# Performance work log

Hardware: AMD Instinct MI355X
Metric: run time of the kernel (lower is better)

Reference implementation:

```python
import jax, jax.numpy as jnp
import numpy as np

IN_F = 1024
HID_F = 4096
OUT_F = 1024
B = 64
D = 768
SPARSE_RATIO = 0.1


def setup_inputs() -> dict:
    key = jax.random.key(0)
    k_x, k_w1, k_w2, k_b, k_m = jax.random.split(key, 5)
    # x: [batch, tokens(d), in_features(s)]
    x = jax.random.normal(k_x, (B, D, IN_F), dtype=jnp.float32)
    # scale weights like typical init so GELU inputs stay in a sane range
    fc1_w = jax.random.normal(k_w1, (HID_F, IN_F), dtype=jnp.float32) * (1.0 / np.sqrt(IN_F))
    fc2_w = jax.random.normal(k_w2, (OUT_F, HID_F), dtype=jnp.float32) * (1.0 / np.sqrt(HID_F))
    fc2_b = jax.random.normal(k_b, (OUT_F,), dtype=jnp.float32) * 0.02
    sparse_mask = (jax.random.uniform(k_m, (IN_F, OUT_F)) < SPARSE_RATIO).astype(jnp.float32)
    return {"x": x, "fc1_w": fc1_w, "fc2_w": fc2_w, "fc2_b": fc2_b, "sparse_mask": sparse_mask}


def reference(x, fc1_w, fc2_w, fc2_b, sparse_mask):
    # attn_s[s,t] = sum_d fc1_w[d,s] * fc2_w[t,d] + fc2_b[t]   -> [in, out]
    attn = (jnp.einsum('ds,td->st', fc1_w, fc2_w) + fc2_b) * sparse_mask
    # dropout with p=0.0 is the identity
    out = jnp.einsum('bds,st->bdt', x, attn)  # [B, D, out]
    # torch nn.GELU default is the exact (erf) variant
    return jax.nn.gelu(out, approximate=False)
```

## Files before the change

kernel.cpp:

```cpp
#include <hip/hip_runtime.h>
#include <hip/hip_bf16.h>
#include <math.h>

typedef __attribute__((ext_vector_type(8))) short  short8;
typedef __attribute__((ext_vector_type(4))) float  floatx4;

__device__ __forceinline__ ushort f2bf(float f) {
    __hip_bfloat16 hb = __float2bfloat16(f);
    return *(ushort*)&hb;
}
__device__ __forceinline__ short8 pack8(float4 a, float4 b) {
    union { short8 v; ushort u[8]; } r;
    r.u[0] = f2bf(a.x); r.u[1] = f2bf(a.y); r.u[2] = f2bf(a.z); r.u[3] = f2bf(a.w);
    r.u[4] = f2bf(b.x); r.u[5] = f2bf(b.y); r.u[6] = f2bf(b.z); r.u[7] = f2bf(b.w);
    return r.v;
}

typedef __attribute__((address_space(1))) const void* gas1_t;
typedef __attribute__((address_space(3))) void*       las3_t;
__device__ __forceinline__ void gload16(const void* g, void* l) {
    __builtin_amdgcn_global_load_lds((gas1_t)g, (las3_t)l, 16, 0, 0);
}

__global__ __launch_bounds__(256) void k_cvt(const float* __restrict__ in,
                                             ushort* __restrict__ out, int n8) {
    int i = blockIdx.x * 256 + threadIdx.x;
    if (i >= n8) return;
    const float4* p = reinterpret_cast<const float4*>(in) + (size_t)i * 2;
    float4 a = p[0], b = p[1];
    *reinterpret_cast<short8*>(out + (size_t)i * 8) = pack8(a, b);
}

__global__ __launch_bounds__(256) void k_transpose(const float* __restrict__ in,
                                                   ushort* __restrict__ out) {
    __shared__ float sm[64][65];
    const int tid = threadIdx.x;
    const int s0 = blockIdx.x * 64;
    const int d0 = blockIdx.y * 64;
#pragma unroll
    for (int i = 0; i < 4; ++i) {
        int lin = i * 256 + tid;
        int dr  = lin >> 4;
        int sc4 = lin & 15;
        float4 v = *reinterpret_cast<const float4*>(&in[(size_t)(d0 + dr) * 1024 + s0 + sc4 * 4]);
        sm[dr][sc4 * 4 + 0] = v.x; sm[dr][sc4 * 4 + 1] = v.y;
        sm[dr][sc4 * 4 + 2] = v.z; sm[dr][sc4 * 4 + 3] = v.w;
    }
    __syncthreads();
#pragma unroll
    for (int i = 0; i < 8; ++i) {
        int lin = i * 256 + tid;
        int dc2 = lin & 31;
        int sr  = lin >> 5;
        uint lo = (uint)f2bf(sm[dc2 * 2][sr]);
        uint hi = (uint)f2bf(sm[dc2 * 2 + 1][sr]);
        *reinterpret_cast<uint*>(&out[(size_t)(s0 + sr) * 4096 + d0 + dc2 * 2]) = lo | (hi << 16);
    }
}

template <int BM, int BN, int EPI, int SWZ>
__global__ __launch_bounds__(256) void k_gemm_b(const ushort* __restrict__ A,
                                                const ushort* __restrict__ B,
                                                const float* __restrict__ bias,
                                                const float* __restrict__ mask,
                                                void* __restrict__ Cout,
                                                int lda, int ldb, int ksteps) {
    __shared__ ushort As[BM * 32];
    __shared__ ushort Bs[BN * 32];
    const int tid  = threadIdx.x;
    const int wave = tid >> 6, lane = tid & 63;
    const int wm = wave >> 1, wn = wave & 1;
    const int quad = lane >> 4, m16 = lane & 15;

    int bx = blockIdx.x, by = blockIdx.y;
    if (SWZ) {
        const int nx   = gridDim.x;
        const int nwg  = nx * gridDim.y;
        const int orig = by * nx + bx;
        const int cpx  = nwg >> 3;
        const int w    = (orig & 7) * cpx + (orig >> 3);
        bx = w % nx; by = w / nx;
    }
    const int n0 = bx * BN;
    const int m0 = by * BM;

    constexpr int AI = BM / 32;
    constexpr int BJ = BN / 32;
    floatx4 acc[AI][BJ];
    const floatx4 zero = {0.f, 0.f, 0.f, 0.f};
#pragma unroll
    for (int i = 0; i < AI; ++i)
#pragma unroll
        for (int j = 0; j < BJ; ++j) acc[i][j] = zero;

    const int gr = lane >> 2;
    const int gc = (lane & 3) * 8;

    for (int kt = 0; kt < ksteps; ++kt) {
        const int k0 = kt * 32;
        if (kt) __syncthreads();
#pragma unroll
        for (int t = 0; t < BM / 64; ++t) {
            const int r = wave * (BM / 4) + t * 16;
            gload16(&A[(size_t)(m0 + r + gr) * lda + k0 + gc], &As[r * 32]);
        }
#pragma unroll
        for (int t = 0; t < BN / 64; ++t) {
            const int r = wave * (BN / 4) + t * 16;
            gload16(&B[(size_t)(n0 + r + gr) * ldb + k0 + gc], &Bs[r * 32]);
        }
        __syncthreads();

        short8 aF[AI], bF[BJ];
#pragma unroll
        for (int i = 0; i < AI; ++i)
            aF[i] = *reinterpret_cast<const short8*>(&As[(wm * (BM / 2) + i * 16 + m16) * 32 + quad * 8]);
#pragma unroll
        for (int j = 0; j < BJ; ++j)
            bF[j] = *reinterpret_cast<const short8*>(&Bs[(wn * (BN / 2) + j * 16 + m16) * 32 + quad * 8]);
#pragma unroll
        for (int i = 0; i < AI; ++i)
#pragma unroll
            for (int j = 0; j < BJ; ++j)
                acc[i][j] = __builtin_amdgcn_mfma_f32_16x16x32_bf16(aF[i], bF[j], acc[i][j], 0, 0, 0);
    }

#pragma unroll
    for (int i = 0; i < AI; ++i) {
#pragma unroll
        for (int j = 0; j < BJ; ++j) {
            const int col = n0 + wn * (BN / 2) + j * 16 + m16;
            float bv = 0.f;
            if (EPI == 0) bv = bias[col];
#pragma unroll
            for (int rr = 0; rr < 4; ++rr) {
                const int row = m0 + wm * (BM / 2) + i * 16 + quad * 4 + rr;
                float v = acc[i][j][rr];
                if (EPI == 0) {
                    v = (v + bv) * mask[(size_t)row * 1024 + col];
                    ((ushort*)Cout)[(size_t)col * 1024 + row] = f2bf(v);
                } else {
                    float g = 0.5f * v * (1.0f + erff(v * 0.70710678118654752f));
                    ((float*)Cout)[(size_t)row * 1024 + col] = g;
                }
            }
        }
    }
}

__global__ __launch_bounds__(256) void k_gemm_f32a(const float* __restrict__ Af,
                                                   const ushort* __restrict__ B,
                                                   float* __restrict__ Cout,
                                                   int lda, int ldb, int ksteps) {
    __shared__ ushort As[128 * 32];
    __shared__ ushort Bs[128 * 32];
    const int tid  = threadIdx.x;
    const int wave = tid >> 6, lane = tid & 63;
    const int wm = wave >> 1, wn = wave & 1;
    const int quad = lane >> 4, m16 = lane & 15;
    const int n0 = blockIdx.x * 128;
    const int m0 = blockIdx.y * 128;

    floatx4 acc[4][4];
    const floatx4 zero = {0.f, 0.f, 0.f, 0.f};
#pragma unroll
    for (int i = 0; i < 4; ++i)
#pragma unroll
        for (int j = 0; j < 4; ++j) acc[i][j] = zero;

    const int s_r = tid >> 2;
    const int s_c = tid & 3;
    const int gr = lane >> 2;
    const int gc = (lane & 3) * 8;

    for (int kt = 0; kt < ksteps; ++kt) {
        const int k0 = kt * 32;
        const float* r0 = &Af[(size_t)(m0 + s_r) * lda + k0 + s_c * 8];
        const float* r1 = &Af[(size_t)(m0 + 64 + s_r) * lda + k0 + s_c * 8];
        short8 a0 = pack8(*reinterpret_cast<const float4*>(r0), *reinterpret_cast<const float4*>(r0 + 4));
        short8 a1 = pack8(*reinterpret_cast<const float4*>(r1), *reinterpret_cast<const float4*>(r1 + 4));
        __syncthreads();
        *reinterpret_cast<short8*>(&As[(s_r)      * 32 + s_c * 8]) = a0;
        *reinterpret_cast<short8*>(&As[(64 + s_r) * 32 + s_c * 8]) = a1;
#pragma unroll
        for (int t = 0; t < 2; ++t) {
            const int r = wave * 32 + t * 16;
            gload16(&B[(size_t)(n0 + r + gr) * ldb + k0 + gc], &Bs[r * 32]);
        }
        __syncthreads();

        short8 aF[4], bF[4];
#pragma unroll
        for (int i = 0; i < 4; ++i)
            aF[i] = *reinterpret_cast<const short8*>(&As[(wm * 64 + i * 16 + m16) * 32 + quad * 8]);
#pragma unroll
        for (int j = 0; j < 4; ++j)
            bF[j] = *reinterpret_cast<const short8*>(&Bs[(wn * 64 + j * 16 + m16) * 32 + quad * 8]);
#pragma unroll
        for (int i = 0; i < 4; ++i)
#pragma unroll
            for (int j = 0; j < 4; ++j)
                acc[i][j] = __builtin_amdgcn_mfma_f32_16x16x32_bf16(aF[i], bF[j], acc[i][j], 0, 0, 0);
    }

#pragma unroll
    for (int i = 0; i < 4; ++i)
#pragma unroll
        for (int j = 0; j < 4; ++j) {
            const int col = n0 + wn * 64 + j * 16 + m16;
#pragma unroll
            for (int rr = 0; rr < 4; ++rr) {
                const int row = m0 + wm * 64 + i * 16 + quad * 4 + rr;
                float v = acc[i][j][rr];
                Cout[(size_t)row * 1024 + col] = 0.5f * v * (1.0f + erff(v * 0.70710678118654752f));
            }
        }
}

extern "C" void kernel_launch(void* const* d_in, const int* in_sizes, int n_in,
                              void* d_out, int out_size, void* d_ws, size_t ws_size,
                              hipStream_t stream) {
    const float* x    = (const float*)d_in[0];
    const float* fc1w = (const float*)d_in[1];
    const float* fc2w = (const float*)d_in[2];
    const float* fc2b = (const float*)d_in[3];
    const float* mask = (const float*)d_in[4];

    char* ws = (char*)d_ws;
    ushort* fc1T  = (ushort*)ws;
    ushort* fc2wb = (ushort*)(ws + (8u  << 20));
    ushort* attnT = (ushort*)(ws + (16u << 20));
    ushort* xb    = (ushort*)(ws + (18u << 20));
    const size_t XB_BYTES = 50331648ull * 2;
    const bool has_xb = ws_size >= (size_t)(18u << 20) + XB_BYTES;

    k_transpose<<<dim3(16, 64), 256, 0, stream>>>(fc1w, fc1T);
    k_cvt<<<2048, 256, 0, stream>>>(fc2w, fc2wb, 524288);
    k_gemm_b<64, 64, 0, 1><<<dim3(16, 16), 256, 0, stream>>>(
        fc1T, fc2wb, fc2b, mask, attnT, 4096, 4096, 128);
    if (has_xb) {
        k_cvt<<<24576, 256, 0, stream>>>(x, xb, 6291456);
        k_gemm_b<128, 128, 1, 1><<<dim3(8, 384), 256, 0, stream>>>(
            xb, attnT, nullptr, nullptr, d_out, 1024, 1024, 32);
    } else {
        k_gemm_f32a<<<dim3(8, 384), 256, 0, stream>>>(x, attnT, (float*)d_out, 1024, 1024, 32);
    }
}
```

Measured before the change: 559.9 us.

## Split-K the attn GEMM and add a pipelined 256x256 main GEMM kernel

The small attn GEMM (K=4096, only 256 blocks) becomes a 4-way split-K with a separate reduction kernel that applies bias, mask and the transpose to bf16, so more of the GPU is busy. The main x@attn GEMM is replaced with a 512-thread kernel that uses 256x256 tiles, swizzled LDS, double-buffered global_load_lds staging, and hand-scheduled barriers, waitcnts and setprio so loads overlap with MFMA. This adds an fp32 partial buffer round trip and a fragile hand pipeline in exchange for higher MFMA utilisation.

```diff
diff --git a/kernel.cpp b/kernel.cpp
--- a/kernel.cpp
+++ b/kernel.cpp
@@ -4,6 +4,7 @@
 
 typedef __attribute__((ext_vector_type(8))) short  short8;
 typedef __attribute__((ext_vector_type(4))) float  floatx4;
+typedef __attribute__((ext_vector_type(4))) int    i32x4;
 
 __device__ __forceinline__ ushort f2bf(float f) {
     __hip_bfloat16 hb = __float2bfloat16(f);
@@ -20,6 +21,11 @@
 typedef __attribute__((address_space(3))) void*       las3_t;
 __device__ __forceinline__ void gload16(const void* g, void* l) {
     __builtin_amdgcn_global_load_lds((gas1_t)g, (las3_t)l, 16, 0, 0);
+}
+__device__ __forceinline__ short8 ds_read16(uint off) {
+    union { i32x4 i; short8 s; } u;
+    asm volatile("ds_read_b128 %0, %1" : "=v"(u.i) : "v"(off));
+    return u.s;
 }
 
 __global__ __launch_bounds__(256) void k_cvt(const float* __restrict__ in,
@@ -72,6 +78,13 @@
     const int wm = wave >> 1, wn = wave & 1;
     const int quad = lane >> 4, m16 = lane & 15;
 
+    if (EPI == 2) {
+        const int sp = blockIdx.z;
+        A += (size_t)sp * 1024;
+        B += (size_t)sp * 1024;
+        Cout = (void*)((float*)Cout + (size_t)sp * 1048576);
+    }
+
     int bx = blockIdx.x, by = blockIdx.y;
     if (SWZ) {
         const int nx   = gridDim.x;
@@ -139,10 +152,161 @@
                 if (EPI == 0) {
                     v = (v + bv) * mask[(size_t)row * 1024 + col];
                     ((ushort*)Cout)[(size_t)col * 1024 + row] = f2bf(v);
-                } else {
+                } else if (EPI == 1) {
                     float g = 0.5f * v * (1.0f + erff(v * 0.70710678118654752f));
                     ((float*)Cout)[(size_t)row * 1024 + col] = g;
+                } else {
+                    ((float*)Cout)[(size_t)col * 1024 + row] = v;
                 }
+            }
+        }
+    }
+}
+
+__global__ __launch_bounds__(256) void k_attn_fin(const float* __restrict__ P,
+                                                  const float* __restrict__ bias,
+                                                  const float* __restrict__ mask,
+                                                  ushort* __restrict__ attnT) {
+    const int idx = blockIdx.x * 256 + threadIdx.x;
+    const int t  = idx >> 7;
+    const int s0 = (idx & 127) << 3;
+    float s[8];
+#pragma unroll
+    for (int j = 0; j < 8; ++j) s[j] = 0.f;
+#pragma unroll
+    for (int sp = 0; sp < 4; ++sp) {
+        const float4* p = reinterpret_cast<const float4*>(&P[(size_t)sp * 1048576 + (size_t)t * 1024 + s0]);
+        float4 a = p[0], b = p[1];
+        s[0] += a.x; s[1] += a.y; s[2] += a.z; s[3] += a.w;
+        s[4] += b.x; s[5] += b.y; s[6] += b.z; s[7] += b.w;
+    }
+    const float bv = bias[t];
+    union { short8 v; ushort u[8]; } r;
+#pragma unroll
+    for (int j = 0; j < 8; ++j) {
+        float v = (s[j] + bv) * mask[(size_t)(s0 + j) * 1024 + t];
+        r.u[j] = f2bf(v);
+    }
+    *reinterpret_cast<short8*>(&attnT[(size_t)t * 1024 + s0]) = r.v;
+}
+
+#define GPH(T_, C_, KS_, MH_, RDB_, NB_)                                         \
+  do {                                                                           \
+    _Pragma("unroll")                                                            \
+    for (int i_ = 0; i_ < 4; ++i_)                                               \
+      aA[i_] = ds_read16(bA_ + (uint)((KS_) * 16384 + ((MH_) * 4 + i_) * 1024)); \
+    if (RDB_) {                                                                  \
+      _Pragma("unroll")                                                          \
+      for (int j_ = 0; j_ < 4; ++j_)                                             \
+        bB[j_] = ds_read16(bB_ + (uint)((KS_) * 16384 + j_ * 1024));             \
+    }                                                                            \
+    stage_ht(4 * (T_) + (C_) + 5);                                               \
+    __builtin_amdgcn_sched_barrier(0);                                           \
+    __builtin_amdgcn_s_barrier();                                                \
+    asm volatile("s_waitcnt lgkmcnt(0)");                                        \
+    __builtin_amdgcn_sched_barrier(0);                                           \
+    __builtin_amdgcn_s_setprio(1);                                               \
+    _Pragma("unroll")                                                            \
+    for (int i_ = 0; i_ < 4; ++i_) {                                             \
+      _Pragma("unroll")                                                          \
+      for (int j_ = 0; j_ < 4; ++j_)                                             \
+        acc[(MH_) * 4 + i_][j_] = __builtin_amdgcn_mfma_f32_16x16x32_bf16(       \
+            aA[i_], bB[j_], acc[(MH_) * 4 + i_][j_], 0, 0, 0);                   \
+    }                                                                            \
+    __builtin_amdgcn_s_setprio(0);                                               \
+    __builtin_amdgcn_sched_barrier(0);                                           \
+    if ((NB_) >= 0) {                                                            \
+      if ((NB_) == 4) asm volatile("s_waitcnt vmcnt(4)");                        \
+      else            asm volatile("s_waitcnt vmcnt(0)");                        \
+      __builtin_amdgcn_sched_barrier(0);                                         \
+    }                                                                            \
+    __builtin_amdgcn_s_barrier();                                                \
+    __builtin_amdgcn_sched_barrier(0);                                           \
+  } while (0)
+
+__global__ __launch_bounds__(512) void k_gemm8(const ushort* __restrict__ A,
+                                               const ushort* __restrict__ B,
+                                               float* __restrict__ C) {
+    constexpr int NT = 16;
+    __shared__ __align__(16) ushort lds[65536];
+
+    const int tid  = threadIdx.x;
+    const int wave = tid >> 6, lane = tid & 63;
+    const int wm = wave >> 2, wn = wave & 3;
+    const int quad = lane >> 4, m16 = lane & 15;
+
+    const int orig = blockIdx.y * 4 + blockIdx.x;
+    const int wsz  = (orig & 7) * 96 + (orig >> 3);
+    const int n0 = (wsz & 3) * 256;
+    const int m0 = (wsz >> 2) * 256;
+
+    const uint lds0 = (uint)(size_t)(las3_t)(void*)lds;
+    const uint xorM = (uint)((m16 & 6) << 3);
+    const uint baseA = lds0 + ((((uint)(wm * 128 + m16)) * 64u + (uint)quad * 16u) ^ xorM);
+    const uint baseB = lds0 + 32768u + ((((uint)(wn * 64 + m16)) * 64u + (uint)quad * 16u) ^ xorM);
+
+    const int srow   = lane >> 2;
+    const int schunk = (((lane & 3) ^ ((lane >> 3) & 3)) << 3);
+
+    auto stage_ht = [&](int g) {
+        if (g >= 4 * NT) return;
+        const int tg = g >> 2, ig = g & 3;
+        const int mat = ig & 1, ks = ig >> 1;
+        const int kc  = tg * 64 + ks * 32 + schunk;
+        const uint dst0 = (uint)(((tg & 1) << 16) | (mat << 15) | (ks << 14));
+        const ushort* src = mat ? B : A;
+        const int r0 = (mat ? n0 : m0) + srow;
+#pragma unroll
+        for (int e = 0; e < 2; ++e) {
+            const int s = e * 8 + wave;
+            gload16(&src[(size_t)(r0 + s * 16) * 1024 + kc],
+                    (void*)((char*)lds + dst0 + (uint)(s << 10)));
+        }
+    };
+
+    floatx4 acc[8][4];
+    const floatx4 zf = {0.f, 0.f, 0.f, 0.f};
+#pragma unroll
+    for (int i = 0; i < 8; ++i)
+#pragma unroll
+        for (int j = 0; j < 4; ++j) acc[i][j] = zf;
+    short8 aA[4], bB[4];
+
+#pragma unroll
+    for (int g = 0; g < 6; ++g) stage_ht(g);
+    asm volatile("s_waitcnt vmcnt(4)");
+    __builtin_amdgcn_sched_barrier(0);
+    __builtin_amdgcn_s_barrier();
+    __builtin_amdgcn_sched_barrier(0);
+
+    for (int tp = 0; tp < NT / 2; ++tp) {
+        const int t0 = 2 * tp, t1 = 2 * tp + 1;
+        {
+            const uint bA_ = baseA, bB_ = baseB;
+            GPH(t0, 1, 0, 0, 1, -1);
+            GPH(t0, 2, 0, 1, 0, -1);
+            GPH(t0, 3, 1, 0, 1, -1);
+            GPH(t0, 4, 1, 1, 0, (tp < 7) ? 4 : 0);
+        }
+        {
+            const uint bA_ = baseA + 65536u, bB_ = baseB + 65536u;
+            GPH(t1, 1, 0, 0, 1, -1);
+            GPH(t1, 2, 0, 1, 0, -1);
+            GPH(t1, 3, 1, 0, 1, -1);
+            GPH(t1, 4, 1, 1, 0, (tp < 7) ? 4 : -1);
+        }
+    }
+
+#pragma unroll
+    for (int mf = 0; mf < 8; ++mf) {
+#pragma unroll
+        for (int nf = 0; nf < 4; ++nf) {
+            const int col = n0 + wn * 64 + nf * 16 + m16;
+#pragma unroll
+            for (int rr = 0; rr < 4; ++rr) {
+                const int row = m0 + wm * 128 + mf * 16 + quad * 4 + rr;
+                const float v = acc[mf][nf][rr];
+                C[(size_t)row * 1024 + col] = 0.5f * v * (1.0f + erff(v * 0.70710678118654752f));
             }
         }
     }
@@ -230,18 +394,27 @@
     ushort* fc1T  = (ushort*)ws;
     ushort* fc2wb = (ushort*)(ws + (8u  << 20));
     ushort* attnT = (ushort*)(ws + (16u << 20));
+    float*  attnP = (float*)(ws + (18u << 20));
     ushort* xb    = (ushort*)(ws + (18u << 20));
     const size_t XB_BYTES = 50331648ull * 2;
     const bool has_xb = ws_size >= (size_t)(18u << 20) + XB_BYTES;
+    const bool has_p  = ws_size >= (size_t)(34u << 20);
 
     k_transpose<<<dim3(16, 64), 256, 0, stream>>>(fc1w, fc1T);
     k_cvt<<<2048, 256, 0, stream>>>(fc2w, fc2wb, 524288);
-    k_gemm_b<64, 64, 0, 1><<<dim3(16, 16), 256, 0, stream>>>(
-        fc1T, fc2wb, fc2b, mask, attnT, 4096, 4096, 128);
+
+    if (has_p) {
+        k_gemm_b<64, 64, 2, 1><<<dim3(16, 16, 4), 256, 0, stream>>>(
+            fc1T, fc2wb, nullptr, nullptr, attnP, 4096, 4096, 32);
+        k_attn_fin<<<512, 256, 0, stream>>>(attnP, fc2b, mask, attnT);
+    } else {
+        k_gemm_b<64, 64, 0, 1><<<dim3(16, 16), 256, 0, stream>>>(
+            fc1T, fc2wb, fc2b, mask, attnT, 4096, 4096, 128);
+    }
+
     if (has_xb) {
         k_cvt<<<24576, 256, 0, stream>>>(x, xb, 6291456);
-        k_gemm_b<128, 128, 1, 1><<<dim3(8, 384), 256, 0, stream>>>(
-            xb, attnT, nullptr, nullptr, d_out, 1024, 1024, 32);
+        k_gemm8<<<dim3(4, 192), 512, 0, stream>>>(xb, attnT, (float*)d_out);
     } else {
         k_gemm_f32a<<<dim3(8, 384), 256, 0, stream>>>(x, attnT, (float*)d_out, 1024, 1024, 32);
     }
```

Result: faster. 509.3 us (-9.0%).
